# Optimization experiments

Measured on AMD Instinct MI355X. Metric: run time of the kernel, lower is better.

Reference implementation:

```python
import jax, jax.numpy as jnp
import numpy as np

N = 512
N_IN = 256
N_OUT = 256


def setup_inputs() -> dict:
    key = jax.random.key(0)
    kx, kw = jax.random.split(key)
    x = jax.random.normal(kx, (N, N_IN), dtype=jnp.float32)
    # xavier_normal_ for Linear(2*n_in -> n_out): std = sqrt(2/(fan_in+fan_out))
    std = float(np.sqrt(2.0 / (2 * N_IN + N_OUT)))
    W = jax.random.normal(kw, (N_OUT, 2 * N_IN), dtype=jnp.float32) * std
    b = jnp.full((N_OUT,), 0.1, dtype=jnp.float32)
    return {"x": x, "W": W, "b": b}


def reference(x, W, b):
    n = x.shape[0]
    # sym=True: node2edge keeps exactly the strict upper-triangular pairs (i<j)
    i, j = jnp.triu_indices(n, k=1)          # each [E], E = n(n-1)/2
    edges = jnp.concatenate([x[i], x[j]], axis=-1)   # [E, 2*n_in]
    h = edges @ W.T + b                               # [E, n_out] (nn.Linear)
    # edges2matrix: scatter rows into flat N*N grid at idx = i*n + j
    out = jnp.zeros((n * n, h.shape[1]), dtype=h.dtype).at[i * n + j].set(h)
    out = out.reshape(n, n, -1)
    # sym: x + x.permute(1,0,2)
    return out + out.transpose(1, 0, 2)
```

## Files before the change

kernel.cpp:

```cpp
#include <hip/hip_runtime.h>

#define NN   512
#define NIN  256
#define NOUT 256
#define ROWS_PER_BLOCK 2

__global__ void __launch_bounds__(256) compute_ab_kernel(
    const float* __restrict__ x, const float* __restrict__ W,
    float* __restrict__ A, float* __restrict__ B)
{
    __shared__ __align__(16) float xs[ROWS_PER_BLOCK][NIN];
    const int t  = threadIdx.x;
    const int i0 = blockIdx.x * ROWS_PER_BLOCK;

    for (int r = 0; r < ROWS_PER_BLOCK; ++r)
        xs[r][t] = x[(i0 + r) * NIN + t];
    __syncthreads();

    float acc_a[ROWS_PER_BLOCK];
    float acc_b[ROWS_PER_BLOCK];
    #pragma unroll
    for (int r = 0; r < ROWS_PER_BLOCK; ++r) { acc_a[r] = 0.f; acc_b[r] = 0.f; }

    const float4* Wrow = reinterpret_cast<const float4*>(W + (size_t)t * (2 * NIN));

    #pragma unroll 4
    for (int k4 = 0; k4 < NIN / 4; ++k4) {
        const float4 wa = Wrow[k4];
        const float4 wb = Wrow[NIN / 4 + k4];
        #pragma unroll
        for (int r = 0; r < ROWS_PER_BLOCK; ++r) {
            const float4 xv = *reinterpret_cast<const float4*>(&xs[r][k4 * 4]);
            acc_a[r] = fmaf(wa.x, xv.x, acc_a[r]);
            acc_a[r] = fmaf(wa.y, xv.y, acc_a[r]);
            acc_a[r] = fmaf(wa.z, xv.z, acc_a[r]);
            acc_a[r] = fmaf(wa.w, xv.w, acc_a[r]);
            acc_b[r] = fmaf(wb.x, xv.x, acc_b[r]);
            acc_b[r] = fmaf(wb.y, xv.y, acc_b[r]);
            acc_b[r] = fmaf(wb.z, xv.z, acc_b[r]);
            acc_b[r] = fmaf(wb.w, xv.w, acc_b[r]);
        }
    }

    for (int r = 0; r < ROWS_PER_BLOCK; ++r) {
        A[(i0 + r) * NOUT + t] = acc_a[r];
        B[(i0 + r) * NOUT + t] = acc_b[r];
    }
}

__global__ void __launch_bounds__(256) write_out_kernel(
    const float4* __restrict__ A4, const float4* __restrict__ B4,
    const float4* __restrict__ b4, float4* __restrict__ out4)
{
    const int total  = NN * NN * (NOUT / 4);
    const int stride = gridDim.x * blockDim.x;
    const int e0     = blockIdx.x * blockDim.x + threadIdx.x;
    const int o4     = e0 & (NOUT / 4 - 1);
    const float4 bv  = b4[o4];

    for (int e = e0; e < total; e += stride) {
        const int j = (e >> 6) & (NN - 1);
        const int i = e >> 15;
        float4 v;
        if (i == j) {
            v = make_float4(0.f, 0.f, 0.f, 0.f);
        } else {
            const int p = i < j ? i : j;
            const int q = i < j ? j : i;
            const float4 a  = A4[p * (NOUT / 4) + o4];
            const float4 bb = B4[q * (NOUT / 4) + o4];
            v = make_float4(a.x + bb.x + bv.x,
                            a.y + bb.y + bv.y,
                            a.z + bb.z + bv.z,
                            a.w + bb.w + bv.w);
        }
        out4[e] = v;
    }
}

extern "C" void kernel_launch(void* const* d_in, const int* in_sizes, int n_in,
                              void* d_out, int out_size, void* d_ws, size_t ws_size,
                              hipStream_t stream) {
    const float* x = (const float*)d_in[0];
    const float* W = (const float*)d_in[1];
    const float* b = (const float*)d_in[2];

    float* A = (float*)d_ws;
    float* B = A + NN * NOUT;

    compute_ab_kernel<<<NN / ROWS_PER_BLOCK, 256, 0, stream>>>(x, W, A, B);
    write_out_kernel<<<2048, 256, 0, stream>>>(
        (const float4*)A, (const float4*)B, (const float4*)b, (float4*)d_out);
}
```

Before: 280.8 us.

## Write symmetric output pairs once per computed edge and fold bias into A

The output writer now assigns each block a balanced pair of rows (i and N-1-i) and loops over j>i, computing each edge value once and storing it to both (i,j) and (j,i), with a separate diagonal zero store. The bias is added into A in the first kernel, so the writer no longer loads it. The first kernel now handles one row per block instead of two, which doubles the W reads. The transposed (j,i) stores are strided, and the work per thread varies with the triangle, so bandwidth efficiency may drop.

```diff
diff --git a/kernel.cpp b/kernel.cpp
--- a/kernel.cpp
+++ b/kernel.cpp
@@ -3,78 +3,64 @@
 #define NN   512
 #define NIN  256
 #define NOUT 256
-#define ROWS_PER_BLOCK 2
+#define NO4  (NOUT / 4)
 
 __global__ void __launch_bounds__(256) compute_ab_kernel(
     const float* __restrict__ x, const float* __restrict__ W,
+    const float* __restrict__ b,
     float* __restrict__ A, float* __restrict__ B)
 {
-    __shared__ __align__(16) float xs[ROWS_PER_BLOCK][NIN];
-    const int t  = threadIdx.x;
-    const int i0 = blockIdx.x * ROWS_PER_BLOCK;
-
-    for (int r = 0; r < ROWS_PER_BLOCK; ++r)
-        xs[r][t] = x[(i0 + r) * NIN + t];
+    __shared__ __align__(16) float xs[NIN];
+    const int t = threadIdx.x;
+    const int i = blockIdx.x;
+    xs[t] = x[i * NIN + t];
     __syncthreads();
 
-    float acc_a[ROWS_PER_BLOCK];
-    float acc_b[ROWS_PER_BLOCK];
-    #pragma unroll
-    for (int r = 0; r < ROWS_PER_BLOCK; ++r) { acc_a[r] = 0.f; acc_b[r] = 0.f; }
-
     const float4* Wrow = reinterpret_cast<const float4*>(W + (size_t)t * (2 * NIN));
-
-    #pragma unroll 4
+    float aa = 0.f, bb = 0.f;
+    #pragma unroll 8
     for (int k4 = 0; k4 < NIN / 4; ++k4) {
         const float4 wa = Wrow[k4];
         const float4 wb = Wrow[NIN / 4 + k4];
-        #pragma unroll
-        for (int r = 0; r < ROWS_PER_BLOCK; ++r) {
-            const float4 xv = *reinterpret_cast<const float4*>(&xs[r][k4 * 4]);
-            acc_a[r] = fmaf(wa.x, xv.x, acc_a[r]);
-            acc_a[r] = fmaf(wa.y, xv.y, acc_a[r]);
-            acc_a[r] = fmaf(wa.z, xv.z, acc_a[r]);
-            acc_a[r] = fmaf(wa.w, xv.w, acc_a[r]);
-            acc_b[r] = fmaf(wb.x, xv.x, acc_b[r]);
-            acc_b[r] = fmaf(wb.y, xv.y, acc_b[r]);
-            acc_b[r] = fmaf(wb.z, xv.z, acc_b[r]);
-            acc_b[r] = fmaf(wb.w, xv.w, acc_b[r]);
-        }
+        const float4 xv = *reinterpret_cast<const float4*>(&xs[k4 * 4]);
+        aa = fmaf(wa.x, xv.x, aa); aa = fmaf(wa.y, xv.y, aa);
+        aa = fmaf(wa.z, xv.z, aa); aa = fmaf(wa.w, xv.w, aa);
+        bb = fmaf(wb.x, xv.x, bb); bb = fmaf(wb.y, xv.y, bb);
+        bb = fmaf(wb.z, xv.z, bb); bb = fmaf(wb.w, xv.w, bb);
     }
-
-    for (int r = 0; r < ROWS_PER_BLOCK; ++r) {
-        A[(i0 + r) * NOUT + t] = acc_a[r];
-        B[(i0 + r) * NOUT + t] = acc_b[r];
-    }
+    A[i * NOUT + t] = aa + b[t];
+    B[i * NOUT + t] = bb;
 }
 
 __global__ void __launch_bounds__(256) write_out_kernel(
     const float4* __restrict__ A4, const float4* __restrict__ B4,
-    const float4* __restrict__ b4, float4* __restrict__ out4)
+    float4* __restrict__ out4)
 {
-    const int total  = NN * NN * (NOUT / 4);
-    const int stride = gridDim.x * blockDim.x;
-    const int e0     = blockIdx.x * blockDim.x + threadIdx.x;
-    const int o4     = e0 & (NOUT / 4 - 1);
-    const float4 bv  = b4[o4];
+    const int t     = threadIdx.x;
+    const int o4    = t & (NO4 - 1);
+    const int g     = t >> 6;
+    const int pair  = blockIdx.x >> 1;
+    const int jhalf = blockIdx.x & 1;
 
-    for (int e = e0; e < total; e += stride) {
-        const int j = (e >> 6) & (NN - 1);
-        const int i = e >> 15;
-        float4 v;
-        if (i == j) {
-            v = make_float4(0.f, 0.f, 0.f, 0.f);
-        } else {
-            const int p = i < j ? i : j;
-            const int q = i < j ? j : i;
-            const float4 a  = A4[p * (NOUT / 4) + o4];
-            const float4 bb = B4[q * (NOUT / 4) + o4];
-            v = make_float4(a.x + bb.x + bv.x,
-                            a.y + bb.y + bv.y,
-                            a.z + bb.z + bv.z,
-                            a.w + bb.w + bv.w);
+    const int rows[2] = { pair, NN - 1 - pair };
+
+    if (jhalf == 0 && g < 2) {
+        const int i = rows[g];
+        out4[((size_t)i * NN + i) * NO4 + o4] = make_float4(0.f, 0.f, 0.f, 0.f);
+    }
+
+    #pragma unroll
+    for (int r = 0; r < 2; ++r) {
+        const int i = rows[r];
+        const float4 a = A4[i * NO4 + o4];
+        #pragma unroll 4
+        for (int j = i + 1 + g + 4 * jhalf; j < NN; j += 8) {
+            const float4 bb = B4[j * NO4 + o4];
+            const float4 v = make_float4(a.x + bb.x, a.y + bb.y,
+                                         a.z + bb.z, a.w + bb.w);
+            out4[((size_t)i * NN + j) * NO4 + o4] = v;
+            out4[((size_t)j * NN + i) * NO4 + o4] = v;
         }
-        out4[e] = v;
     }
 }
 
@@ -88,7 +74,7 @@
     float* A = (float*)d_ws;
     float* B = A + NN * NOUT;
 
-    compute_ab_kernel<<<NN / ROWS_PER_BLOCK, 256, 0, stream>>>(x, W, A, B);
-    write_out_kernel<<<2048, 256, 0, stream>>>(
-        (const float4*)A, (const float4*)B, (const float4*)b, (float4*)d_out);
+    compute_ab_kernel<<<NN, 256, 0, stream>>>(x, W, b, A, B);
+    write_out_kernel<<<NN, 256, 0, stream>>>(
+        (const float4*)A, (const float4*)B, (float4*)d_out);
 }
```

After: 294.3 us. 4.8% more time.
